# Optimization experiments

Hardware: AMD Instinct MI355X
Metric: run time of the kernel (lower is better)

Reference implementation:

```python
import jax, jax.numpy as jnp
import numpy as np

MODEL_DIM = 1024
NUM_HEADS = 16
D_K = MODEL_DIM // NUM_HEADS  # 64
MAX_SEQ_LEN = 3200
B, T = 2, 2048
THETA_BASE = 10000.0


def setup_inputs() -> dict:
    key = jax.random.key(0)
    ks = jax.random.split(key, 5)
    scale = 1.0 / np.sqrt(MODEL_DIM)
    x = jax.random.normal(ks[0], (B, T, MODEL_DIM), dtype=jnp.float32)
    wq = jax.random.normal(ks[1], (MODEL_DIM, MODEL_DIM), dtype=jnp.float32) * scale
    wk = jax.random.normal(ks[2], (MODEL_DIM, MODEL_DIM), dtype=jnp.float32) * scale
    wv = jax.random.normal(ks[3], (MODEL_DIM, MODEL_DIM), dtype=jnp.float32) * scale
    wo = jax.random.normal(ks[4], (MODEL_DIM, MODEL_DIM), dtype=jnp.float32) * scale
    bq = jnp.zeros((MODEL_DIM,), jnp.float32)
    bk = jnp.zeros((MODEL_DIM,), jnp.float32)
    bv = jnp.zeros((MODEL_DIM,), jnp.float32)
    bo = jnp.zeros((MODEL_DIM,), jnp.float32)
    # RoPE tables, exactly as precompute_rotation_matrix: theta duplicated
    # adjacently ([t0,t0,t1,t1,...]).
    theta = THETA_BASE ** (jnp.arange(D_K // 2, dtype=jnp.float32) * (-2.0 / D_K))
    ang = jnp.outer(jnp.arange(MAX_SEQ_LEN, dtype=jnp.float32), theta)  # [L, d/2]
    ang = jnp.repeat(ang, 2, axis=-1)  # [L, d]
    return {
        "x": x, "wq": wq, "bq": bq, "wk": wk, "bk": bk,
        "wv": wv, "bv": bv, "wo": wo, "bo": bo,
        "cos": jnp.cos(ang), "sin": jnp.sin(ang),
    }


def reference(x, wq, bq, wk, bk, wv, bv, wo, bo, cos, sin):
    b, t, dm = x.shape
    h, d = NUM_HEADS, dm // NUM_HEADS

    # NOTE: original uses .view(b, h, t, d) directly on [b, t, h*d] (no
    # transpose) — a nonstandard head split we replicate faithfully.
    xq = (x @ wq.T + bq).reshape(b, h, t, d)
    xk = (x @ wk.T + bk).reshape(b, h, t, d)
    xv = (x @ wv.T + bv).reshape(b, h, t, d)

    def rot_half(q):
        # pairs are adjacent (2i, 2i+1): out[2i] = -q[2i+1], out[2i+1] = q[2i]
        q2 = q.reshape(b, h, t, d // 2, 2)
        return jnp.stack([-q2[..., 1], q2[..., 0]], axis=-1).reshape(b, h, t, d)

    # NOTE: original indexes cos/sin at the single position `seq_len`
    # (rotation_matrix_cos[:, :, xq.shape[2], :]), broadcasting one row over
    # all positions — replicated faithfully.
    c = cos[t]  # [d]
    s = sin[t]  # [d]
    xq = xq * c + rot_half(xq) * s
    xk = xk * c + rot_half(xk) * s

    scores = jnp.einsum("bhqd,bhkd->bhqk", xq, xk) / np.sqrt(d)
    p = jax.nn.softmax(scores, axis=-1)  # mask='none', dropout=0.0
    o = jnp.einsum("bhqk,bhkd->bhqd", p, xv)
    o = o.transpose(0, 2, 1, 3).reshape(b, t, dm)  # 'b h t d -> b t (h d)'
    return o @ wo.T + bo
```

## Files before the change

kernel.cpp:

```cpp
#include <hip/hip_runtime.h>

typedef _Float16 half8 __attribute__((ext_vector_type(8)));
typedef __fp16 pkh2 __attribute__((ext_vector_type(2)));
typedef float floatx4 __attribute__((ext_vector_type(4)));

#define AS1 __attribute__((address_space(1)))
#define AS3 __attribute__((address_space(3)))


__global__ __launch_bounds__(256) void convert_kernel(
    const float* __restrict__ x, const float* __restrict__ wq,
    const float* __restrict__ wk, const float* __restrict__ wv,
    const float* __restrict__ wo,
    _Float16* __restrict__ xb, _Float16* __restrict__ wqkv,
    _Float16* __restrict__ wob)
{
    int i = (blockIdx.x * 256 + threadIdx.x) * 4;
    const float* src; _Float16* dst; int off;
    if (i < 4194304)      { src = x;  dst = xb;            off = i; }
    else if (i < 5242880) { src = wq; dst = wqkv;          off = i - 4194304; }
    else if (i < 6291456) { src = wk; dst = wqkv + 1048576; off = i - 5242880; }
    else if (i < 7340032) { src = wv; dst = wqkv + 2097152; off = i - 6291456; }
    else                  { src = wo; dst = wob;           off = i - 7340032; }
    float4 v = *(const float4*)(src + off);
    union { uint2 u; pkh2 h[2]; } o;
    o.h[0] = __builtin_amdgcn_cvt_pkrtz(v.x, v.y);
    o.h[1] = __builtin_amdgcn_cvt_pkrtz(v.z, v.w);
    *(uint2*)(dst + off) = o.u;
}

template<bool QKV>
__global__ __launch_bounds__(256) void gemm_kernel(
    const _Float16* __restrict__ A, const _Float16* __restrict__ W,
    const float* __restrict__ b0, const float* __restrict__ b1,
    const float* __restrict__ b2,
    const float* __restrict__ cosr, const float* __restrict__ sinr,
    _Float16* __restrict__ O0, _Float16* __restrict__ O1,
    _Float16* __restrict__ O2, float* __restrict__ Of)
{
    __shared__ __align__(16) _Float16 As[128 * 64];
    __shared__ __align__(16) _Float16 Bs[128 * 64];
    const int tid  = threadIdx.x;
    const int lane = tid & 63, w = tid >> 6;
    const int lrow = lane & 15, quad = lane >> 4;
    const int wr = (w & 1) * 64, wc = (w >> 1) * 64;
    const int arow0 = blockIdx.x * 128;
    const int brow0 = blockIdx.y * 128;

    const int r8 = lane >> 3;
    const int gcol = ((lane & 7) ^ r8) * 8;

    floatx4 acc[4][4] = {};

    for (int kk = 0; kk < 1024; kk += 64) {
        __syncthreads();
        for (int u = 0; u < 4; u++) {
            const int row = w * 32 + u * 8;
            __builtin_amdgcn_global_load_lds(
                (const AS1 unsigned*)(const void*)(A + (size_t)(arow0 + row + r8) * 1024 + kk + gcol),
                (AS3 unsigned*)(void*)(As + row * 64), 16, 0, 0);
            __builtin_amdgcn_global_load_lds(
                (const AS1 unsigned*)(const void*)(W + (size_t)(brow0 + row + r8) * 1024 + kk + gcol),
                (AS3 unsigned*)(void*)(Bs + row * 64), 16, 0, 0);
        }
        __syncthreads();
        for (int ks = 0; ks < 2; ks++) {
            const int swz = ((ks * 4 + quad) ^ (lrow & 7)) * 8;
            half8 af[4], bf[4];
            for (int mt = 0; mt < 4; mt++)
                af[mt] = *(const half8*)&As[(wr + mt * 16 + lrow) * 64 + swz];
            for (int nt = 0; nt < 4; nt++)
                bf[nt] = *(const half8*)&Bs[(wc + nt * 16 + lrow) * 64 + swz];
            for (int mt = 0; mt < 4; mt++)
                for (int nt = 0; nt < 4; nt++)
                    acc[mt][nt] = __builtin_amdgcn_mfma_f32_16x16x32_f16(
                        af[mt], bf[nt], acc[mt][nt], 0, 0, 0);
        }
    }

    if (QKV) {
        const int seg = blockIdx.y >> 3;
        const float* bias = seg == 0 ? b0 : (seg == 1 ? b1 : b2);
        _Float16* out = seg == 0 ? O0 : (seg == 1 ? O1 : O2);
        const int nbase = (blockIdx.y & 7) * 128 + wc;
        for (int nt = 0; nt < 4; nt++) {
            const int n = nbase + nt * 16 + lrow;
            const float bv = bias[n];
            const int dj = n & 63;
            const float cv = cosr[dj], sv = sinr[dj];
            const bool odd = (n & 1) != 0;
            for (int mt = 0; mt < 4; mt++)
                for (int r = 0; r < 4; r++) {
                    float v = acc[mt][nt][r] + bv;
                    if (seg < 2) {
                        float p = __shfl_xor(v, 1, 64);
                        v = odd ? (v * cv + p * sv) : (v * cv - p * sv);
                    }
                    if (seg == 0) v *= 0.125f;
                    int row = arow0 + wr + mt * 16 + quad * 4 + r;
                    out[row * 1024 + n] = (_Float16)v;
                }
        }
    } else {
        const int nbase = blockIdx.y * 128 + wc;
        for (int nt = 0; nt < 4; nt++) {
            const int n = nbase + nt * 16 + lrow;
            const float bv = b0[n];
            for (int mt = 0; mt < 4; mt++)
                for (int r = 0; r < 4; r++) {
                    int row = arow0 + wr + mt * 16 + quad * 4 + r;
                    Of[row * 1024 + n] = acc[mt][nt][r] + bv;
                }
        }
    }
}

__global__ __launch_bounds__(256) void vtrans_kernel(
    const _Float16* __restrict__ V, _Float16* __restrict__ VT)
{
    __shared__ __align__(16) _Float16 T[64][72];
    const int tid = threadIdx.x;
    const int kt = blockIdx.x;
    const int bh = blockIdx.y;
    const int bi = bh >> 4, hi = bh & 15;
    const _Float16* Vh = V + (size_t)(bi * 2048 + hi * 128) * 1024 + kt * 4096;
    const int srow = tid >> 3, sblk = tid & 7;
    union { uint4 u; _Float16 h[8]; } a, b;
    a.u = *(const uint4*)(Vh + (2 * srow) * 64 + sblk * 8);
    b.u = *(const uint4*)(Vh + (2 * srow + 1) * 64 + sblk * 8);
    for (int j = 0; j < 8; j++) {
        union { unsigned u; _Float16 h[2]; } pk;
        pk.h[0] = a.h[j]; pk.h[1] = b.h[j];
        *(unsigned*)&T[sblk * 8 + j][2 * srow] = pk.u;
    }
    __syncthreads();
    const int d = tid >> 2, c = tid & 3;
    _Float16* out = VT + ((size_t)bh * 64 + d) * 2048 + kt * 64 + c * 16;
    *(uint4*)(out)     = *(const uint4*)&T[d][c * 16];
    *(uint4*)(out + 8) = *(const uint4*)&T[d][c * 16 + 8];
}

__global__ __launch_bounds__(256, 3) void attn_kernel(
    const _Float16* __restrict__ Q, const _Float16* __restrict__ K,
    const _Float16* __restrict__ VT, _Float16* __restrict__ O)
{
    __shared__ __align__(16) _Float16 Ks[2][64][72];
    __shared__ __align__(16) _Float16 Vts[2][64][72];
    __shared__ __align__(16) _Float16 Pt[4][32][40];

    const int tid  = threadIdx.x;
    const int lane = tid & 63, w = tid >> 6;
    const int lrow = lane & 15, quad = lane >> 4;
    const int qt = blockIdx.x, bh = blockIdx.y;
    const int bi = bh >> 4, hi = bh & 15;
    const size_t base = (size_t)(bi * 2048 + hi * 128) * 1024;
    const _Float16* Qh  = Q + base;
    const _Float16* Kh  = K + base;
    const _Float16* VTh = VT + (size_t)bh * 131072;

    half8 qf[2][2];
    for (int nt = 0; nt < 2; nt++)
        for (int ks = 0; ks < 2; ks++)
            qf[nt][ks] = *(const half8*)(Qh + (qt * 128 + w * 32 + nt * 16 + lrow) * 64
                                          + ks * 32 + quad * 8);

    floatx4 oacc[4][2] = {};
    float lsum0 = 0.0f, lsum1 = 0.0f;

    const int srow = tid >> 3, sblk = tid & 7;
    const int vd = tid >> 2, vc = tid & 3;

    {
        *(uint4*)&Ks[0][srow][sblk * 8]      = *(const uint4*)(Kh + srow * 64 + sblk * 8);
        *(uint4*)&Ks[0][srow + 32][sblk * 8] = *(const uint4*)(Kh + (srow + 32) * 64 + sblk * 8);
        const _Float16* vsrc = VTh + (size_t)vd * 2048 + vc * 16;
        *(uint4*)&Vts[0][vd][vc * 16]     = *(const uint4*)(vsrc);
        *(uint4*)&Vts[0][vd][vc * 16 + 8] = *(const uint4*)(vsrc + 8);
    }
    __syncthreads();

    const float LOG2E = 1.44269504f;
    const float OFF   = -8.65617025f;

    for (int kt = 0; kt < 32; kt++) {
        const int cur = kt & 1;
        uint4 k0, k1, v0, v1;
        if (kt < 31) {
            const _Float16* Kt = Kh + (kt + 1) * 4096;
            const _Float16* Vt = VTh + (size_t)vd * 2048 + (kt + 1) * 64 + vc * 16;
            k0 = *(const uint4*)(Kt + srow * 64 + sblk * 8);
            k1 = *(const uint4*)(Kt + (srow + 32) * 64 + sblk * 8);
            v0 = *(const uint4*)(Vt);
            v1 = *(const uint4*)(Vt + 8);
        }
        for (int h = 0; h < 2; h++) {
            for (int k2 = 0; k2 < 2; k2++) {
                const int kt4 = h * 2 + k2;
                floatx4 s0 = {}, s1 = {};
                for (int ks = 0; ks < 2; ks++) {
                    half8 af = *(const half8*)&Ks[cur][kt4 * 16 + lrow][ks * 32 + quad * 8];
                    s0 = __builtin_amdgcn_mfma_f32_16x16x32_f16(af, qf[0][ks], s0, 0, 0, 0);
                    s1 = __builtin_amdgcn_mfma_f32_16x16x32_f16(af, qf[1][ks], s1, 0, 0, 0);
                }
                float p00 = __builtin_amdgcn_exp2f(fmaf(s0[0], LOG2E, OFF));
                float p01 = __builtin_amdgcn_exp2f(fmaf(s0[1], LOG2E, OFF));
                float p02 = __builtin_amdgcn_exp2f(fmaf(s0[2], LOG2E, OFF));
                float p03 = __builtin_amdgcn_exp2f(fmaf(s0[3], LOG2E, OFF));
                float p10 = __builtin_amdgcn_exp2f(fmaf(s1[0], LOG2E, OFF));
                float p11 = __builtin_amdgcn_exp2f(fmaf(s1[1], LOG2E, OFF));
                float p12 = __builtin_amdgcn_exp2f(fmaf(s1[2], LOG2E, OFF));
                float p13 = __builtin_amdgcn_exp2f(fmaf(s1[3], LOG2E, OFF));
                lsum0 += p00 + p01 + p02 + p03;
                lsum1 += p10 + p11 + p12 + p13;
                union { uint2 u; pkh2 h2[2]; } pk0, pk1;
                pk0.h2[0] = __builtin_amdgcn_cvt_pkrtz(p00, p01);
                pk0.h2[1] = __builtin_amdgcn_cvt_pkrtz(p02, p03);
                pk1.h2[0] = __builtin_amdgcn_cvt_pkrtz(p10, p11);
                pk1.h2[1] = __builtin_amdgcn_cvt_pkrtz(p12, p13);
                *(uint2*)&Pt[w][lrow][k2 * 16 + quad * 4]      = pk0.u;
                *(uint2*)&Pt[w][16 + lrow][k2 * 16 + quad * 4] = pk1.u;
            }
            half8 bf0 = *(const half8*)&Pt[w][lrow][quad * 8];
            half8 bf1 = *(const half8*)&Pt[w][16 + lrow][quad * 8];
            for (int dt = 0; dt < 4; dt++) {
                half8 av = *(const half8*)&Vts[cur][dt * 16 + lrow][h * 32 + quad * 8];
                oacc[dt][0] = __builtin_amdgcn_mfma_f32_16x16x32_f16(av, bf0, oacc[dt][0], 0, 0, 0);
                oacc[dt][1] = __builtin_amdgcn_mfma_f32_16x16x32_f16(av, bf1, oacc[dt][1], 0, 0, 0);
            }
        }
        if (kt < 31) {
            const int nxt = cur ^ 1;
            *(uint4*)&Ks[nxt][srow][sblk * 8]      = k0;
            *(uint4*)&Ks[nxt][srow + 32][sblk * 8] = k1;
            *(uint4*)&Vts[nxt][vd][vc * 16]     = v0;
            *(uint4*)&Vts[nxt][vd][vc * 16 + 8] = v1;
        }
        __syncthreads();
    }

    lsum0 += __shfl_xor(lsum0, 16, 64); lsum0 += __shfl_xor(lsum0, 32, 64);
    lsum1 += __shfl_xor(lsum1, 16, 64); lsum1 += __shfl_xor(lsum1, 32, 64);
    const float inv0 = 1.0f / lsum0, inv1 = 1.0f / lsum1;
    _Float16* Es = (_Float16*)Ks + w * 2304;
    for (int dt = 0; dt < 4; dt++) {
        union { uint2 u; pkh2 h2[2]; } a0, a1;
        a0.h2[0] = __builtin_amdgcn_cvt_pkrtz(oacc[dt][0][0] * inv0, oacc[dt][0][1] * inv0);
        a0.h2[1] = __builtin_amdgcn_cvt_pkrtz(oacc[dt][0][2] * inv0, oacc[dt][0][3] * inv0);
        a1.h2[0] = __builtin_amdgcn_cvt_pkrtz(oacc[dt][1][0] * inv1, oacc[dt][1][1] * inv1);
        a1.h2[1] = __builtin_amdgcn_cvt_pkrtz(oacc[dt][1][2] * inv1, oacc[dt][1][3] * inv1);
        *(uint2*)&Es[lrow * 72 + dt * 16 + quad * 4]        = a0.u;
        *(uint2*)&Es[(16 + lrow) * 72 + dt * 16 + quad * 4] = a1.u;
    }
    const int rw = lane >> 1, hf = lane & 1;
    const size_t orow = (size_t)(bi * 2048 + qt * 128 + w * 32 + rw) * 1024
                        + hi * 64 + hf * 32;
    for (int i = 0; i < 4; i++)
        *(uint4*)(O + orow + i * 8) = *(const uint4*)&Es[rw * 72 + hf * 32 + i * 8];
}

extern "C" void kernel_launch(void* const* d_in, const int* in_sizes, int n_in,
                              void* d_out, int out_size, void* d_ws, size_t ws_size,
                              hipStream_t stream) {
    const float* x    = (const float*)d_in[0];
    const float* wq   = (const float*)d_in[1];
    const float* bq   = (const float*)d_in[2];
    const float* wk   = (const float*)d_in[3];
    const float* bk   = (const float*)d_in[4];
    const float* wv   = (const float*)d_in[5];
    const float* bv   = (const float*)d_in[6];
    const float* wo   = (const float*)d_in[7];
    const float* bo   = (const float*)d_in[8];
    const float* cosT = (const float*)d_in[9];
    const float* sinT = (const float*)d_in[10];

    _Float16* ws   = (_Float16*)d_ws;
    _Float16* xb   = ws;
    _Float16* wqkv = xb + 4194304;
    _Float16* wob  = wqkv + 3145728;
    _Float16* Qb   = wob + 1048576;
    _Float16* Kb   = Qb + 4194304;
    _Float16* Vb   = Kb + 4194304;
    _Float16* Ob   = Vb + 4194304;
    _Float16* VTb  = xb;

    convert_kernel<<<8192, 256, 0, stream>>>(x, wq, wk, wv, wo, xb, wqkv, wob);
    gemm_kernel<true><<<dim3(32, 24), 256, 0, stream>>>(
        xb, wqkv, bq, bk, bv, cosT + 2048 * 64, sinT + 2048 * 64,
        Qb, Kb, Vb, nullptr);
    vtrans_kernel<<<dim3(32, 32), 256, 0, stream>>>(Vb, VTb);
    attn_kernel<<<dim3(16, 32), 256, 0, stream>>>(Qb, Kb, VTb, Ob);
    gemm_kernel<false><<<dim3(32, 8), 256, 0, stream>>>(
        Ob, wob, bo, nullptr, nullptr, nullptr, nullptr,
        nullptr, nullptr, nullptr, (float*)d_out);
}
```

Measured before the change: 216.3 us.

## Split attention KV range across two warp groups and feed P via registers

```diff
diff --git a/kernel.cpp b/kernel.cpp
--- a/kernel.cpp
+++ b/kernel.cpp
@@ -1,6 +1,7 @@
 #include <hip/hip_runtime.h>
 
 typedef _Float16 half8 __attribute__((ext_vector_type(8)));
+typedef _Float16 half4 __attribute__((ext_vector_type(4)));
 typedef __fp16 pkh2 __attribute__((ext_vector_type(2)));
 typedef float floatx4 __attribute__((ext_vector_type(4)));
 
@@ -140,23 +141,27 @@
     *(uint4*)(out + 8) = *(const uint4*)&T[d][c * 16 + 8];
 }
 
-__global__ __launch_bounds__(256, 3) void attn_kernel(
+__global__ __launch_bounds__(512, 4) void attn_kernel(
     const _Float16* __restrict__ Q, const _Float16* __restrict__ K,
     const _Float16* __restrict__ VT, _Float16* __restrict__ O)
 {
-    __shared__ __align__(16) _Float16 Ks[2][64][72];
-    __shared__ __align__(16) _Float16 Vts[2][64][72];
-    __shared__ __align__(16) _Float16 Pt[4][32][40];
+    __shared__ __align__(16) _Float16 Ks[2][2][64][72];
+    __shared__ __align__(16) _Float16 Vts[2][2][64][72];
 
     const int tid  = threadIdx.x;
-    const int lane = tid & 63, w = tid >> 6;
+    const int g    = tid >> 8;
+    const int t8   = tid & 255;
+    const int lane = tid & 63, w = (tid >> 6) & 3;
     const int lrow = lane & 15, quad = lane >> 4;
-    const int qt = blockIdx.x, bh = blockIdx.y;
+
+    const int bid = blockIdx.x;
+    const int bh  = (bid & 7) * 4 + (bid >> 7);
+    const int qt  = (bid >> 3) & 15;
     const int bi = bh >> 4, hi = bh & 15;
     const size_t base = (size_t)(bi * 2048 + hi * 128) * 1024;
     const _Float16* Qh  = Q + base;
-    const _Float16* Kh  = K + base;
-    const _Float16* VTh = VT + (size_t)bh * 131072;
+    const _Float16* Kh  = K + base + (size_t)g * 65536;
+    const _Float16* VTh = VT + (size_t)bh * 131072 + g * 1024;
 
     half8 qf[2][2];
     for (int nt = 0; nt < 2; nt++)
@@ -167,95 +172,105 @@
     floatx4 oacc[4][2] = {};
     float lsum0 = 0.0f, lsum1 = 0.0f;
 
-    const int srow = tid >> 3, sblk = tid & 7;
-    const int vd = tid >> 2, vc = tid & 3;
+    const int srow = t8 >> 3, sblk = t8 & 7;
+    const int vd = t8 >> 2, vc = t8 & 3;
+    const _Float16* vbase = VTh + (size_t)vd * 2048 + vc * 16;
 
     {
-        *(uint4*)&Ks[0][srow][sblk * 8]      = *(const uint4*)(Kh + srow * 64 + sblk * 8);
-        *(uint4*)&Ks[0][srow + 32][sblk * 8] = *(const uint4*)(Kh + (srow + 32) * 64 + sblk * 8);
-        const _Float16* vsrc = VTh + (size_t)vd * 2048 + vc * 16;
-        *(uint4*)&Vts[0][vd][vc * 16]     = *(const uint4*)(vsrc);
-        *(uint4*)&Vts[0][vd][vc * 16 + 8] = *(const uint4*)(vsrc + 8);
+        *(uint4*)&Ks[g][0][srow][sblk * 8]      = *(const uint4*)(Kh + srow * 64 + sblk * 8);
+        *(uint4*)&Ks[g][0][srow + 32][sblk * 8] = *(const uint4*)(Kh + (srow + 32) * 64 + sblk * 8);
+        *(uint4*)&Vts[g][0][vd][vc * 16]     = *(const uint4*)(vbase);
+        *(uint4*)&Vts[g][0][vd][vc * 16 + 8] = *(const uint4*)(vbase + 8);
     }
     __syncthreads();
 
     const float LOG2E = 1.44269504f;
     const float OFF   = -8.65617025f;
 
-    for (int kt = 0; kt < 32; kt++) {
-        const int cur = kt & 1;
+    for (int ktl = 0; ktl < 16; ktl++) {
+        const int cur = ktl & 1;
         uint4 k0, k1, v0, v1;
-        if (kt < 31) {
-            const _Float16* Kt = Kh + (kt + 1) * 4096;
-            const _Float16* Vt = VTh + (size_t)vd * 2048 + (kt + 1) * 64 + vc * 16;
+        if (ktl < 15) {
+            const _Float16* Kt = Kh + (ktl + 1) * 4096;
+            const _Float16* Vt = vbase + (ktl + 1) * 64;
             k0 = *(const uint4*)(Kt + srow * 64 + sblk * 8);
             k1 = *(const uint4*)(Kt + (srow + 32) * 64 + sblk * 8);
             v0 = *(const uint4*)(Vt);
             v1 = *(const uint4*)(Vt + 8);
         }
-        for (int h = 0; h < 2; h++) {
-            for (int k2 = 0; k2 < 2; k2++) {
-                const int kt4 = h * 2 + k2;
-                floatx4 s0 = {}, s1 = {};
-                for (int ks = 0; ks < 2; ks++) {
-                    half8 af = *(const half8*)&Ks[cur][kt4 * 16 + lrow][ks * 32 + quad * 8];
-                    s0 = __builtin_amdgcn_mfma_f32_16x16x32_f16(af, qf[0][ks], s0, 0, 0, 0);
-                    s1 = __builtin_amdgcn_mfma_f32_16x16x32_f16(af, qf[1][ks], s1, 0, 0, 0);
-                }
-                float p00 = __builtin_amdgcn_exp2f(fmaf(s0[0], LOG2E, OFF));
-                float p01 = __builtin_amdgcn_exp2f(fmaf(s0[1], LOG2E, OFF));
-                float p02 = __builtin_amdgcn_exp2f(fmaf(s0[2], LOG2E, OFF));
-                float p03 = __builtin_amdgcn_exp2f(fmaf(s0[3], LOG2E, OFF));
-                float p10 = __builtin_amdgcn_exp2f(fmaf(s1[0], LOG2E, OFF));
-                float p11 = __builtin_amdgcn_exp2f(fmaf(s1[1], LOG2E, OFF));
-                float p12 = __builtin_amdgcn_exp2f(fmaf(s1[2], LOG2E, OFF));
-                float p13 = __builtin_amdgcn_exp2f(fmaf(s1[3], LOG2E, OFF));
-                lsum0 += p00 + p01 + p02 + p03;
-                lsum1 += p10 + p11 + p12 + p13;
-                union { uint2 u; pkh2 h2[2]; } pk0, pk1;
-                pk0.h2[0] = __builtin_amdgcn_cvt_pkrtz(p00, p01);
-                pk0.h2[1] = __builtin_amdgcn_cvt_pkrtz(p02, p03);
-                pk1.h2[0] = __builtin_amdgcn_cvt_pkrtz(p10, p11);
-                pk1.h2[1] = __builtin_amdgcn_cvt_pkrtz(p12, p13);
-                *(uint2*)&Pt[w][lrow][k2 * 16 + quad * 4]      = pk0.u;
-                *(uint2*)&Pt[w][16 + lrow][k2 * 16 + quad * 4] = pk1.u;
+        for (int kt4 = 0; kt4 < 4; kt4++) {
+            floatx4 s0 = {}, s1 = {};
+            for (int ks = 0; ks < 2; ks++) {
+                half8 af = *(const half8*)&Ks[g][cur][kt4 * 16 + lrow][ks * 32 + quad * 8];
+                s0 = __builtin_amdgcn_mfma_f32_16x16x32_f16(af, qf[0][ks], s0, 0, 0, 0);
+                s1 = __builtin_amdgcn_mfma_f32_16x16x32_f16(af, qf[1][ks], s1, 0, 0, 0);
             }
-            half8 bf0 = *(const half8*)&Pt[w][lrow][quad * 8];
-            half8 bf1 = *(const half8*)&Pt[w][16 + lrow][quad * 8];
+            float p00 = __builtin_amdgcn_exp2f(fmaf(s0[0], LOG2E, OFF));
+            float p01 = __builtin_amdgcn_exp2f(fmaf(s0[1], LOG2E, OFF));
+            float p02 = __builtin_amdgcn_exp2f(fmaf(s0[2], LOG2E, OFF));
+            float p03 = __builtin_amdgcn_exp2f(fmaf(s0[3], LOG2E, OFF));
+            float p10 = __builtin_amdgcn_exp2f(fmaf(s1[0], LOG2E, OFF));
+            float p11 = __builtin_amdgcn_exp2f(fmaf(s1[1], LOG2E, OFF));
+            float p12 = __builtin_amdgcn_exp2f(fmaf(s1[2], LOG2E, OFF));
+            float p13 = __builtin_amdgcn_exp2f(fmaf(s1[3], LOG2E, OFF));
+            lsum0 += (p00 + p01) + (p02 + p03);
+            lsum1 += (p10 + p11) + (p12 + p13);
+            union { half4 h4; pkh2 h2[2]; } pk0, pk1;
+            pk0.h2[0] = __builtin_amdgcn_cvt_pkrtz(p00, p01);
+            pk0.h2[1] = __builtin_amdgcn_cvt_pkrtz(p02, p03);
+            pk1.h2[0] = __builtin_amdgcn_cvt_pkrtz(p10, p11);
+            pk1.h2[1] = __builtin_amdgcn_cvt_pkrtz(p12, p13);
             for (int dt = 0; dt < 4; dt++) {
-                half8 av = *(const half8*)&Vts[cur][dt * 16 + lrow][h * 32 + quad * 8];
-                oacc[dt][0] = __builtin_amdgcn_mfma_f32_16x16x32_f16(av, bf0, oacc[dt][0], 0, 0, 0);
-                oacc[dt][1] = __builtin_amdgcn_mfma_f32_16x16x32_f16(av, bf1, oacc[dt][1], 0, 0, 0);
+                half4 av = *(const half4*)&Vts[g][cur][dt * 16 + lrow][kt4 * 16 + quad * 4];
+                oacc[dt][0] = __builtin_amdgcn_mfma_f32_16x16x16f16(av, pk0.h4, oacc[dt][0], 0, 0, 0);
+                oacc[dt][1] = __builtin_amdgcn_mfma_f32_16x16x16f16(av, pk1.h4, oacc[dt][1], 0, 0, 0);
             }
         }
-        if (kt < 31) {
+        if (ktl < 15) {
             const int nxt = cur ^ 1;
-            *(uint4*)&Ks[nxt][srow][sblk * 8]      = k0;
-            *(uint4*)&Ks[nxt][srow + 32][sblk * 8] = k1;
-            *(uint4*)&Vts[nxt][vd][vc * 16]     = v0;
-            *(uint4*)&Vts[nxt][vd][vc * 16 + 8] = v1;
+            *(uint4*)&Ks[g][nxt][srow][sblk * 8]      = k0;
+            *(uint4*)&Ks[g][nxt][srow + 32][sblk * 8] = k1;
+            *(uint4*)&Vts[g][nxt][vd][vc * 16]     = v0;
+            *(uint4*)&Vts[g][nxt][vd][vc * 16 + 8] = v1;
         }
         __syncthreads();
     }
 
-    lsum0 += __shfl_xor(lsum0, 16, 64); lsum0 += __shfl_xor(lsum0, 32, 64);
-    lsum1 += __shfl_xor(lsum1, 16, 64); lsum1 += __shfl_xor(lsum1, 32, 64);
-    const float inv0 = 1.0f / lsum0, inv1 = 1.0f / lsum1;
-    _Float16* Es = (_Float16*)Ks + w * 2304;
-    for (int dt = 0; dt < 4; dt++) {
-        union { uint2 u; pkh2 h2[2]; } a0, a1;
-        a0.h2[0] = __builtin_amdgcn_cvt_pkrtz(oacc[dt][0][0] * inv0, oacc[dt][0][1] * inv0);
-        a0.h2[1] = __builtin_amdgcn_cvt_pkrtz(oacc[dt][0][2] * inv0, oacc[dt][0][3] * inv0);
-        a1.h2[0] = __builtin_amdgcn_cvt_pkrtz(oacc[dt][1][0] * inv1, oacc[dt][1][1] * inv1);
-        a1.h2[1] = __builtin_amdgcn_cvt_pkrtz(oacc[dt][1][2] * inv1, oacc[dt][1][3] * inv1);
-        *(uint2*)&Es[lrow * 72 + dt * 16 + quad * 4]        = a0.u;
-        *(uint2*)&Es[(16 + lrow) * 72 + dt * 16 + quad * 4] = a1.u;
-    }
-    const int rw = lane >> 1, hf = lane & 1;
-    const size_t orow = (size_t)(bi * 2048 + qt * 128 + w * 32 + rw) * 1024
-                        + hi * 64 + hf * 32;
-    for (int i = 0; i < 4; i++)
-        *(uint4*)(O + orow + i * 8) = *(const uint4*)&Es[rw * 72 + hf * 32 + i * 8];
+    float* X = (float*)&Ks[0][0][0][0];
+    float* L = (float*)&Vts[1][0][0][0];
+    if (g == 1) {
+        for (int dt = 0; dt < 4; dt++)
+            for (int nt = 0; nt < 2; nt++)
+                *(floatx4*)&X[((dt * 2 + nt) * 256 + w * 64 + lane) * 4] = oacc[dt][nt];
+        L[(w * 64 + lane) * 2]     = lsum0;
+        L[(w * 64 + lane) * 2 + 1] = lsum1;
+    }
+    __syncthreads();
+    if (g == 0) {
+        for (int dt = 0; dt < 4; dt++)
+            for (int nt = 0; nt < 2; nt++)
+                oacc[dt][nt] += *(const floatx4*)&X[((dt * 2 + nt) * 256 + w * 64 + lane) * 4];
+        lsum0 += L[(w * 64 + lane) * 2];
+        lsum1 += L[(w * 64 + lane) * 2 + 1];
+        lsum0 += __shfl_xor(lsum0, 16, 64); lsum0 += __shfl_xor(lsum0, 32, 64);
+        lsum1 += __shfl_xor(lsum1, 16, 64); lsum1 += __shfl_xor(lsum1, 32, 64);
+        const float inv0 = 1.0f / lsum0, inv1 = 1.0f / lsum1;
+        _Float16* Es = &Vts[0][0][0][0] + w * 2304;
+        for (int dt = 0; dt < 4; dt++) {
+            union { uint2 u; pkh2 h2[2]; } a0, a1;
+            a0.h2[0] = __builtin_amdgcn_cvt_pkrtz(oacc[dt][0][0] * inv0, oacc[dt][0][1] * inv0);
+            a0.h2[1] = __builtin_amdgcn_cvt_pkrtz(oacc[dt][0][2] * inv0, oacc[dt][0][3] * inv0);
+            a1.h2[0] = __builtin_amdgcn_cvt_pkrtz(oacc[dt][1][0] * inv1, oacc[dt][1][1] * inv1);
+            a1.h2[1] = __builtin_amdgcn_cvt_pkrtz(oacc[dt][1][2] * inv1, oacc[dt][1][3] * inv1);
+            *(uint2*)&Es[lrow * 72 + dt * 16 + quad * 4]        = a0.u;
+            *(uint2*)&Es[(16 + lrow) * 72 + dt * 16 + quad * 4] = a1.u;
+        }
+        const int rw = lane >> 1, hf = lane & 1;
+        const size_t orow = (size_t)(bi * 2048 + qt * 128 + w * 32 + rw) * 1024
+                            + hi * 64 + hf * 32;
+        for (int i = 0; i < 4; i++)
+            *(uint4*)(O + orow + i * 8) = *(const uint4*)&Es[rw * 72 + hf * 32 + i * 8];
+    }
 }
 
 extern "C" void kernel_launch(void* const* d_in, const int* in_sizes, int n_in,
@@ -288,7 +303,7 @@
         xb, wqkv, bq, bk, bv, cosT + 2048 * 64, sinT + 2048 * 64,
         Qb, Kb, Vb, nullptr);
     vtrans_kernel<<<dim3(32, 32), 256, 0, stream>>>(Vb, VTb);
-    attn_kernel<<<dim3(16, 32), 256, 0, stream>>>(Qb, Kb, VTb, Ob);
+    attn_kernel<<<dim3(512), 512, 0, stream>>>(Qb, Kb, VTb, Ob);
     gemm_kernel<false><<<dim3(32, 8), 256, 0, stream>>>(
         Ob, wob, bo, nullptr, nullptr, nullptr, nullptr,
         nullptr, nullptr, nullptr, (float*)d_out);
```

After: 226.0 us. +4.5%, slower.
